# Performance work log

Measured on AMD Instinct MI355X. Metric: run time of the kernel, lower is better.

## Reference

```python
import jax, jax.numpy as jnp
import numpy as np

LN_EPS = 1e-5
ROPE_BASE = 10000.0


def rotate_half(x):
    # x: [..., d]; split into two halves (matches einops '(j d)->j d', j=2)
    d2 = x.shape[-1] // 2
    x1, x2 = x[..., :d2], x[..., d2:]
    return jnp.concatenate((-x2, x1), axis=-1)


def rotary_pos_emb(n, head_dim, dtype=jnp.float32):
    inv_freq = 1.0 / (ROPE_BASE ** (jnp.arange(0, head_dim, 2, dtype=jnp.float32) / head_dim))
    t = jnp.arange(n, dtype=jnp.float32)
    freqs = jnp.einsum('i,j->ij', t, inv_freq)          # [n, d/2]
    return jnp.concatenate((freqs, freqs), axis=-1).astype(dtype)  # [n, d]


def apply_rotary(pos, t):
    return t * jnp.cos(pos) + rotate_half(t) * jnp.sin(pos)


def setup_inputs() -> dict:
    key = jax.random.key(0)
    ks = jax.random.split(key, 4)
    b, n, dm = 2, 4096, 2048
    x = jax.random.normal(ks[0], (b, n, dm), dtype=jnp.float32)
    wq = jax.random.normal(ks[1], (dm, dm), dtype=jnp.float32) * (dm ** -0.5)
    wk = jax.random.normal(ks[2], (dm, dm), dtype=jnp.float32) * (dm ** -0.5)
    wv = jax.random.normal(ks[3], (dm, dm), dtype=jnp.float32) * (dm ** -0.5)
    return {
        'x': x,
        'ln_gamma': jnp.ones((dm,), jnp.float32),
        'ln_beta': jnp.zeros((dm,), jnp.float32),
        'wq': wq, 'wk': wk, 'wv': wv,
        'num_heads': 16,
    }


def reference(x, ln_gamma, ln_beta, wq, wk, wv, num_heads):
    b, n, dm = x.shape
    hd = dm // num_heads
    # LayerNorm (eps=1e-5, torch default)
    mu = jnp.mean(x, axis=-1, keepdims=True)
    var = jnp.mean(jnp.square(x - mu), axis=-1, keepdims=True)
    xn = (x - mu) * jax.lax.rsqrt(var + LN_EPS) * ln_gamma + ln_beta
    # QKV projections (nn.Linear, bias=False => x @ W.T; weights stored as [out,in])
    q = jnp.einsum('bnd,ed->bne', xn, wq)
    k = jnp.einsum('bnd,ed->bne', xn, wk)
    v = jnp.einsum('bnd,ed->bne', xn, wv)
    # b n (h d) -> b h n d
    split = lambda t: t.reshape(b, n, num_heads, hd).transpose(0, 2, 1, 3)
    q, k, v = split(q), split(k), split(v)
    pos = rotary_pos_emb(n, hd, x.dtype)  # [n, hd], broadcasts over b,h
    q = apply_rotary(pos, q)
    k = apply_rotary(pos, k)
    return q, k, v
```

## Files before the change

### kernel.cpp

```cpp
#include <hip/hip_runtime.h>
#include <hip/hip_bf16.h>


typedef float f32x4 __attribute__((ext_vector_type(4)));
typedef __bf16 bf16x8 __attribute__((ext_vector_type(8)));
typedef __bf16 bf16x4 __attribute__((ext_vector_type(4)));

#define DM    2048
#define NSEQ  4096
#define NH    16
#define HD    128
#define NROWS 8192
#define MAT_ELEMS (2ull*NH*NSEQ*HD)

typedef __attribute__((address_space(1))) const void GV;
typedef __attribute__((address_space(3))) void LV;
__device__ __forceinline__ void gload_lds16(const void* g, void* l) {
    __builtin_amdgcn_global_load_lds((GV*)g, (LV*)l, 16, 0, 0);
}

__global__ __launch_bounds__(256)
void lncvt_kernel(const float* __restrict__ x, const float* __restrict__ g,
                  const float* __restrict__ be,
                  const float* __restrict__ wq, const float* __restrict__ wk,
                  const float* __restrict__ wv,
                  __bf16* __restrict__ xnb, __bf16* __restrict__ wb) {
    int bid = blockIdx.x;
    int tid = threadIdx.x;
    if (bid < NROWS) {
        int row = bid;
        const float4* xr = (const float4*)(x + (size_t)row * DM);
        float4 v0 = xr[tid];
        float4 v1 = xr[tid + 256];
        float s  = v0.x + v0.y + v0.z + v0.w + v1.x + v1.y + v1.z + v1.w;
        float ss = v0.x*v0.x + v0.y*v0.y + v0.z*v0.z + v0.w*v0.w
                 + v1.x*v1.x + v1.y*v1.y + v1.z*v1.z + v1.w*v1.w;
#pragma unroll
        for (int o = 32; o > 0; o >>= 1) {
            s  += __shfl_down(s, o);
            ss += __shfl_down(ss, o);
        }
        __shared__ float red[10];
        int wave = tid >> 6, lane = tid & 63;
        if (lane == 0) { red[wave] = s; red[4 + wave] = ss; }
        __syncthreads();
        if (tid == 0) {
            float S  = red[0] + red[1] + red[2] + red[3];
            float SS = red[4] + red[5] + red[6] + red[7];
            float mu  = S * (1.0f / DM);
            float var = SS * (1.0f / DM) - mu * mu;
            red[8] = mu;
            red[9] = rsqrtf(var + 1e-5f);
        }
        __syncthreads();
        float mu = red[8], rs = red[9];

        const float4* gp = (const float4*)g;
        const float4* bp = (const float4*)be;
        bf16x4* orow = (bf16x4*)(xnb + (size_t)row * DM);
        {
            float4 g0 = gp[tid], b0 = bp[tid];
            bf16x4 o;
            o[0] = (__bf16)((v0.x - mu) * rs * g0.x + b0.x);
            o[1] = (__bf16)((v0.y - mu) * rs * g0.y + b0.y);
            o[2] = (__bf16)((v0.z - mu) * rs * g0.z + b0.z);
            o[3] = (__bf16)((v0.w - mu) * rs * g0.w + b0.w);
            orow[tid] = o;
        }
        {
            float4 g1 = gp[tid + 256], b1 = bp[tid + 256];
            bf16x4 o;
            o[0] = (__bf16)((v1.x - mu) * rs * g1.x + b1.x);
            o[1] = (__bf16)((v1.y - mu) * rs * g1.y + b1.y);
            o[2] = (__bf16)((v1.z - mu) * rs * g1.z + b1.z);
            o[3] = (__bf16)((v1.w - mu) * rs * g1.w + b1.w);
            orow[tid + 256] = o;
        }
    } else {
        int cb = bid - NROWS;
        const float* a = (cb < 2048) ? wq : (cb < 4096) ? wk : wv;
        size_t base = ((size_t)(cb & 2047) * 256 + tid) * 8;
        float4 v0 = *(const float4*)(a + base);
        float4 v1 = *(const float4*)(a + base + 4);
        bf16x8 r;
        r[0] = (__bf16)v0.x; r[1] = (__bf16)v0.y; r[2] = (__bf16)v0.z; r[3] = (__bf16)v0.w;
        r[4] = (__bf16)v1.x; r[5] = (__bf16)v1.y; r[6] = (__bf16)v1.z; r[7] = (__bf16)v1.w;
        *(bf16x8*)(wb + (size_t)(cb >> 11) * 4194304 + base) = r;
    }
}


__device__ __forceinline__ void loadA4(bf16x8 (&a)[4][2], const __bf16* Sp,
                                       int base, int mb, int o0) {
#pragma unroll
    for (int mi = 0; mi < 4; mi++)
#pragma unroll
        for (int ks = 0; ks < 2; ks++)
            a[mi][ks] = *(const bf16x8*)(Sp + base + (mb + mi) * 1024 + (o0 ^ (ks * 32)));
}
__device__ __forceinline__ void loadB2(bf16x8 (&b)[2][2], const __bf16* Sp,
                                       int base, int cb, int o0) {
#pragma unroll
    for (int f = 0; f < 2; f++)
#pragma unroll
        for (int ks = 0; ks < 2; ks++)
            b[f][ks] = *(const bf16x8*)(Sp + base + (f * 16 + (cb >> 1) * 64) * 64 + (o0 ^ (ks * 32)));
}

template<int RB, int CB>
__device__ __forceinline__ void cluster(f32x4 (&acc)[8][4], bf16x8 (&a)[4][2],
                                        bf16x8 (&b)[2][2]) {
    __builtin_amdgcn_s_setprio(1);
#pragma unroll
    for (int mi = 0; mi < 4; mi++)
#pragma unroll
        for (int ni = 0; ni < 2; ni++)
#pragma unroll
            for (int ks = 0; ks < 2; ks++)
                acc[RB + mi][CB + ni] = __builtin_amdgcn_mfma_f32_16x16x32_bf16(
                    a[mi][ks], b[ni][ks], acc[RB + mi][CB + ni], 0, 0, 0);
    __builtin_amdgcn_s_setprio(0);
}

#define FENCE asm volatile("" ::: "memory")
#define BAR   do { FENCE; __builtin_amdgcn_s_barrier(); FENCE; } while (0)
#define BARO  do { BAR; asm volatile("s_waitcnt lgkmcnt(0)" ::: "memory"); \
                   __builtin_amdgcn_sched_barrier(0); } while (0)
#define VM6   asm volatile("s_waitcnt vmcnt(6)" ::: "memory")
#define VM0   asm volatile("s_waitcnt vmcnt(0)" ::: "memory")
#define VMX   do {} while (0)

#define STGA(P, kt, HF) do { \
    gload_lds16(pA + (size_t)((HF) * 64 + w * 8) * DM + (kt) * 64,       &As[P][((HF) * 8 + w) * 512]); \
    gload_lds16(pA + (size_t)((HF) * 64 + 128 + w * 8) * DM + (kt) * 64, &As[P][((HF) * 8 + 16 + w) * 512]); \
} while (0)
#define STGB(P, kt, HF) do { \
    gload_lds16(pB + (size_t)((HF) * 64 + w * 8) * DM + (kt) * 64,       &Bs[P][((HF) * 8 + w) * 512]); \
    gload_lds16(pB + (size_t)((HF) * 64 + 128 + w * 8) * DM + (kt) * 64, &Bs[P][((HF) * 8 + 16 + w) * 512]); \
} while (0)

#define KTILE(kt, P, Q, SG0, SG1, SG2, SG3, W3) do { \
     \
    loadA4(a,  &As[P][0], baseA, 0, o0); \
    loadB2(b0, &Bs[P][0], baseB, 0, o0); \
    if (SG0) STGA(Q, (kt) + 1, 1);                \
    BARO; cluster<0, 0>(acc, a, b0); BAR; \
     \
    loadB2(b1, &Bs[P][0], baseB, 2, o0); \
    if (SG1) STGA(P, (kt) + 2, 0);                \
    BARO; cluster<0, 2>(acc, a, b1); BAR; \
     \
    loadA4(a, &As[P][0], baseA, 4, o0); \
    if (SG2) STGB(P, (kt) + 2, 0);                \
    BARO; cluster<4, 2>(acc, a, b1); BAR; \
     \
    if (SG3) STGB(P, (kt) + 2, 1);                \
    W3; \
    BARO; cluster<4, 0>(acc, a, b0); BAR; \
} while (0)

__global__ __launch_bounds__(512, 2)
void gemm_qkv(const __bf16* __restrict__ A,
              const __bf16* __restrict__ Wq,
              const __bf16* __restrict__ Wk,
              const __bf16* __restrict__ Wv,
              float* __restrict__ out) {
    __shared__ __bf16 As[2][16384];
    __shared__ __bf16 Bs[2][16384];

    int tid = threadIdx.x;
    int w = tid >> 6, l = tid & 63;
    int wm = w >> 2, wn = w & 3;

    int bid = blockIdx.x;
    int x = bid & 7;
    int ridx = bid >> 3;
    int q = ridx >> 5;
    int s = ridx & 31;
    int mtp, ntp;
    if (q == 0)      { mtp = s >> 3;       ntp = s & 7; }
    else if (q == 1) { mtp = 4 + (s >> 3); ntp = s & 7; }
    else             { mtp = s & 7;        ntp = 8 + (s >> 3); }
    int mt = (x & 3) * 8 + mtp;
    int nt = (x >> 2) * 12 + ntp;
    int mat = nt >> 3, ntb = nt & 7;
    const __bf16* Wp = (mat == 0) ? Wq : (mat == 1) ? Wk : Wv;
    int row0 = mt * 256, colp = ntb * 256;

    int lr = l >> 3;
    int lco = ((l & 7) ^ lr) * 8;
    const __bf16* pA = A  + (size_t)(row0 + lr) * DM + lco;
    const __bf16* pB = Wp + (size_t)(colp + lr) * DM + lco;

    int baseA = (wm * 128 + (l & 15)) * 64;
    int baseB = ((wn & 1) * 32 + (wn >> 1) * 128 + (l & 15)) * 64;
    int o0 = ((l >> 4) * 8) ^ ((l & 7) * 8);

    STGA(0, 0, 0); STGB(0, 0, 0); STGB(0, 0, 1); STGA(0, 0, 1);
    STGA(1, 1, 0); STGB(1, 1, 0); STGB(1, 1, 1);

    f32x4 acc[8][4];
#pragma unroll
    for (int i = 0; i < 8; i++)
#pragma unroll
        for (int j = 0; j < 4; j++)
            acc[i][j] = (f32x4){0.f, 0.f, 0.f, 0.f};

    bf16x8 a[4][2], b0[2][2], b1[2][2];

    VM6;
    BAR;

#pragma unroll 1
    for (int kt = 0; kt < 30; kt += 2) {
        KTILE(kt,     0, 1, 1, 1, 1, 1, VM6);
        KTILE(kt + 1, 1, 0, 1, 1, 1, 1, VM6);
    }
    KTILE(30, 0, 1, 1, 0, 0, 0, VM0);
    KTILE(31, 1, 0, 0, 0, 0, 0, VMX);

    float* op = out + (size_t)mat * MAT_ELEMS;
    int hd_lo = (wn & 1) * 32 + (l & 15);
    int head = ntb * 2 + (wn >> 1);
    int r_base = row0 + wm * 128 + ((l >> 4) << 2);
    float if0 = exp2f(-0.20762051f * (float)hd_lo);
    float if1 = exp2f(-0.20762051f * (float)(hd_lo + 16));

    if (mat < 2) {
#pragma unroll
        for (int mi = 0; mi < 8; mi++) {
#pragma unroll
            for (int j = 0; j < 4; j++) {
                int r = r_base + mi * 16 + j;
                int b = r >> 12, n = r & 4095;
                float fn = (float)n;
                float* rowp = op + ((size_t)((b * NH + head) * NSEQ + n)) * HD;
#pragma unroll
                for (int ni = 0; ni < 2; ni++) {
                    float lo = acc[mi][ni][j], hi = acc[mi][ni + 2][j];
                    float sv, cv;
                    __sincosf(fn * (ni ? if1 : if0), &sv, &cv);
                    rowp[hd_lo + ni * 16]      = lo * cv - hi * sv;
                    rowp[hd_lo + ni * 16 + 64] = hi * cv + lo * sv;
                }
            }
        }
    } else {
#pragma unroll
        for (int mi = 0; mi < 8; mi++) {
#pragma unroll
            for (int j = 0; j < 4; j++) {
                int r = r_base + mi * 16 + j;
                int b = r >> 12, n = r & 4095;
                float* rowp = op + ((size_t)((b * NH + head) * NSEQ + n)) * HD;
#pragma unroll
                for (int ni = 0; ni < 2; ni++) {
                    rowp[hd_lo + ni * 16]      = acc[mi][ni][j];
                    rowp[hd_lo + ni * 16 + 64] = acc[mi][ni + 2][j];
                }
            }
        }
    }
}

extern "C" void kernel_launch(void* const* d_in, const int* in_sizes, int n_in,
                              void* d_out, int out_size, void* d_ws, size_t ws_size,
                              hipStream_t stream) {
    const float* x  = (const float*)d_in[0];
    const float* g  = (const float*)d_in[1];
    const float* be = (const float*)d_in[2];
    const float* wq = (const float*)d_in[3];
    const float* wk = (const float*)d_in[4];
    const float* wv = (const float*)d_in[5];
    float* out = (float*)d_out;

    char* ws = (char*)d_ws;
    __bf16* xnb = (__bf16*)ws;
    __bf16* wb  = (__bf16*)(ws + 33554432);

    lncvt_kernel<<<NROWS + 6144, 256, 0, stream>>>(x, g, be, wq, wk, wv, xnb, wb);
    gemm_qkv<<<768, 512, 0, stream>>>(xnb, wb, wb + 4194304, wb + 8388608, out);
}
```

Baseline: 221.5 us.

## Replace interleaved 4-phase GEMM k-loop with simple double-buffered prefetch

Restructures the QKV GEMM main loop. Previously each K tile was split into four barrier-separated MFMA clusters, with global-to-LDS loads for upcoming tiles interleaved between them. Now each tile waits on vmcnt, runs one barrier, loads all fragments, issues all MFMA clusters back to back, then issues the whole next-next tile prefetch after a trailing barrier. This cuts the barrier count per tile from eight to two. In exchange it gives up the fine-grained overlap of loads with compute and the explicit lgkmcnt waits and sched barriers.

```diff
diff --git a/kernel.cpp b/kernel.cpp
--- a/kernel.cpp
+++ b/kernel.cpp
@@ -124,11 +124,8 @@
 
 #define FENCE asm volatile("" ::: "memory")
 #define BAR   do { FENCE; __builtin_amdgcn_s_barrier(); FENCE; } while (0)
-#define BARO  do { BAR; asm volatile("s_waitcnt lgkmcnt(0)" ::: "memory"); \
-                   __builtin_amdgcn_sched_barrier(0); } while (0)
-#define VM6   asm volatile("s_waitcnt vmcnt(6)" ::: "memory")
+#define VM8   asm volatile("s_waitcnt vmcnt(8)" ::: "memory")
 #define VM0   asm volatile("s_waitcnt vmcnt(0)" ::: "memory")
-#define VMX   do {} while (0)
 
 #define STGA(P, kt, HF) do { \
     gload_lds16(pA + (size_t)((HF) * 64 + w * 8) * DM + (kt) * 64,       &As[P][((HF) * 8 + w) * 512]); \
@@ -139,24 +136,19 @@
     gload_lds16(pB + (size_t)((HF) * 64 + 128 + w * 8) * DM + (kt) * 64, &Bs[P][((HF) * 8 + 16 + w) * 512]); \
 } while (0)
 
-#define KTILE(kt, P, Q, SG0, SG1, SG2, SG3, W3) do { \
-     \
+#define KTILE(kt, P, SG, W) do { \
+    W; BAR; \
     loadA4(a,  &As[P][0], baseA, 0, o0); \
     loadB2(b0, &Bs[P][0], baseB, 0, o0); \
-    if (SG0) STGA(Q, (kt) + 1, 1);                \
-    BARO; cluster<0, 0>(acc, a, b0); BAR; \
-     \
     loadB2(b1, &Bs[P][0], baseB, 2, o0); \
-    if (SG1) STGA(P, (kt) + 2, 0);                \
-    BARO; cluster<0, 2>(acc, a, b1); BAR; \
-     \
+    cluster<0, 0>(acc, a, b0); \
+    cluster<0, 2>(acc, a, b1); \
     loadA4(a, &As[P][0], baseA, 4, o0); \
-    if (SG2) STGB(P, (kt) + 2, 0);                \
-    BARO; cluster<4, 2>(acc, a, b1); BAR; \
-     \
-    if (SG3) STGB(P, (kt) + 2, 1);                \
-    W3; \
-    BARO; cluster<4, 0>(acc, a, b0); BAR; \
+    cluster<4, 0>(acc, a, b0); \
+    cluster<4, 2>(acc, a, b1); \
+    BAR; \
+    if (SG) { STGA(P, (kt) + 2, 0); STGA(P, (kt) + 2, 1); \
+              STGB(P, (kt) + 2, 0); STGB(P, (kt) + 2, 1); } \
 } while (0)
 
 __global__ __launch_bounds__(512, 2)
@@ -196,8 +188,8 @@
     int baseB = ((wn & 1) * 32 + (wn >> 1) * 128 + (l & 15)) * 64;
     int o0 = ((l >> 4) * 8) ^ ((l & 7) * 8);
 
-    STGA(0, 0, 0); STGB(0, 0, 0); STGB(0, 0, 1); STGA(0, 0, 1);
-    STGA(1, 1, 0); STGB(1, 1, 0); STGB(1, 1, 1);
+    STGA(0, 0, 0); STGA(0, 0, 1); STGB(0, 0, 0); STGB(0, 0, 1);
+    STGA(1, 1, 0); STGA(1, 1, 1); STGB(1, 1, 0); STGB(1, 1, 1);
 
     f32x4 acc[8][4];
 #pragma unroll
@@ -208,16 +200,13 @@
 
     bf16x8 a[4][2], b0[2][2], b1[2][2];
 
-    VM6;
-    BAR;
-
 #pragma unroll 1
     for (int kt = 0; kt < 30; kt += 2) {
-        KTILE(kt,     0, 1, 1, 1, 1, 1, VM6);
-        KTILE(kt + 1, 1, 0, 1, 1, 1, 1, VM6);
+        KTILE(kt,     0, 1, VM8);
+        KTILE(kt + 1, 1, 1, VM8);
     }
-    KTILE(30, 0, 1, 1, 0, 0, 0, VM0);
-    KTILE(31, 1, 0, 0, 0, 0, 0, VMX);
+    KTILE(30, 0, 0, VM8);
+    KTILE(31, 1, 0, VM0);
 
     float* op = out + (size_t)mat * MAT_ELEMS;
     int hd_lo = (wn & 1) * 32 + (l & 15);
```

After: 228.3 us. 1.03x slower.
